# Performance work log

Hardware: AMD Instinct MI355X
Metric: run time of the kernel (lower is better)

Reference implementation:

```python
import jax, jax.numpy as jnp
import numpy as np

KS = 3
N = KS * KS  # 9 kernel taps
EPS = 1e-5
LEAK = 0.1


def _conv2d(x, w, b=None, stride=1, pad=1):
    out = jax.lax.conv_general_dilated(
        x, w, (stride, stride), [(pad, pad), (pad, pad)],
        dimension_numbers=('NCHW', 'OIHW', 'NCHW'))
    if b is not None:
        out = out + b[None, :, None, None]
    return out


def setup_inputs() -> dict:
    key = jax.random.key(0)
    k1, k2, k3, k4 = jax.random.split(key, 4)
    b, c_in, c_out, H, W = 4, 128, 256, 128, 128
    x = jax.random.normal(k1, (b, c_in, H, W), dtype=jnp.float32)
    # offset-predicting conv (torch inits it to zero; small random keeps
    # sampling near-grid but nontrivial)
    p_w = jax.random.normal(k2, (2 * N, c_in, KS, KS), dtype=jnp.float32) * 0.01
    p_b = jnp.zeros((2 * N,), dtype=jnp.float32)
    # main conv weight (bias=False in DeformConv2d)
    w_conv = jax.random.normal(k3, (c_out, c_in, KS, KS), dtype=jnp.float32) * 0.05
    gamma = jnp.ones((c_out,), dtype=jnp.float32)
    beta = jnp.zeros((c_out,), dtype=jnp.float32)
    return {"x": x, "p_w": p_w, "p_b": p_b, "w_conv": w_conv,
            "gamma": gamma, "beta": beta}


def reference(x, p_w, p_b, w_conv, gamma, beta):
    b, c, H, W = x.shape
    # offsets: (b, 2N, H, W); first N channels = x-offsets, last N = y-offsets
    off = jnp.transpose(_conv2d(x, p_w, p_b), (0, 2, 3, 1))  # (b,h,w,2N)
    off_x, off_y = off[..., :N], off[..., N:]

    x_pad = jnp.pad(x, ((0, 0), (0, 0), (1, 1), (1, 1)))  # zero_padding(1)
    Hp, Wp = H + 2, W + 2

    # p = p_0 + p_n + offset (in padded coordinates)
    dx = jnp.repeat(jnp.arange(-1, 2), KS).astype(x.dtype)  # (9,)
    dy = jnp.tile(jnp.arange(-1, 2), KS).astype(x.dtype)
    p0x = jnp.arange(1, H + 1, dtype=x.dtype)[None, :, None, None]
    p0y = jnp.arange(1, W + 1, dtype=x.dtype)[None, None, :, None]
    px = p0x + dx + off_x  # (b,h,w,N)
    py = p0y + dy + off_y

    fx, fy = jnp.floor(px), jnp.floor(py)
    qlt_x = jnp.clip(fx, 0, Hp - 1)
    qlt_y = jnp.clip(fy, 0, Wp - 1)
    qrb_x = jnp.clip(fx + 1, 0, Hp - 1)
    qrb_y = jnp.clip(fy + 1, 0, Wp - 1)

    pcx = jnp.clip(px, 0, Hp - 1)
    pcy = jnp.clip(py, 0, Wp - 1)

    # bilinear weights (matches original g_lt/g_rb/g_lb/g_rt)
    g_lt = (1 + (qlt_x - pcx)) * (1 + (qlt_y - pcy))
    g_rb = (1 - (qrb_x - pcx)) * (1 - (qrb_y - pcy))
    g_lb = (1 + (qlt_x - pcx)) * (1 - (qrb_y - pcy))
    g_rt = (1 - (qrb_x - pcx)) * (1 + (qlt_y - pcy))

    x_flat = x_pad.reshape(b, c, Hp * Wp)
    ilt_x, ilt_y = qlt_x.astype(jnp.int32), qlt_y.astype(jnp.int32)
    irb_x, irb_y = qrb_x.astype(jnp.int32), qrb_y.astype(jnp.int32)

    def samp(ix, iy, g):
        idx = (ix * Wp + iy).reshape(b, -1)  # (b, h*w*N)
        v = jnp.take_along_axis(x_flat, idx[:, None, :], axis=2)
        return g[:, None] * v.reshape(b, c, H, W, N)

    x_off = (samp(ilt_x, ilt_y, g_lt) + samp(irb_x, irb_y, g_rb)
             + samp(ilt_x, irb_y, g_lb) + samp(irb_x, ilt_y, g_rt))

    # equivalent to reshaping to (b,c,3h,3w) and conv(k=3,s=3), bias=False
    out = jnp.einsum('bchwn,ocn->bohw', x_off,
                     w_conv.reshape(w_conv.shape[0], c, N))

    # BatchNorm2d (training-mode batch stats, biased var) + LeakyReLU(0.1)
    mean = out.mean(axis=(0, 2, 3), keepdims=True)
    var = ((out - mean) ** 2).mean(axis=(0, 2, 3), keepdims=True)
    out = (out - mean) * jax.lax.rsqrt(var + EPS)
    out = out * gamma[None, :, None, None] + beta[None, :, None, None]
    return jnp.where(out >= 0, out, LEAK * out)
```

## Files before the change

kernel.cpp:

```cpp
#include <hip/hip_runtime.h>
#include <cstdint>

typedef __attribute__((ext_vector_type(8))) short bf16x8;
typedef __attribute__((ext_vector_type(4))) float f32x4;

#define B_   4
#define C_   128
#define H_   128
#define W_   128
#define HP_  130
#define WP_  130
#define O_   256
#define HW_  (H_*W_)

#define XPAD_BYTES   (B_*HP_*WP_*C_*2)
#define OFF_BYTE     XPAD_BYTES
#define OFF_BYTES    (B_*HW_*18*4)
#define WREPB_BYTE   (OFF_BYTE + OFF_BYTES)
#define WREPB_BYTES  (9*C_*O_*2)
#define STATS_BYTE   (WREPB_BYTE + WREPB_BYTES)
#define WOFF_BYTE    (STATS_BYTE + 4096)
#define WOFF_BYTES   (9*4*4*32*8*2)

typedef __attribute__((address_space(1))) const void gconst_void;
typedef __attribute__((address_space(3))) void lds_void;
#define GLD_LDS16(gp, lp) __builtin_amdgcn_global_load_lds((gconst_void*)(gp), (lds_void*)(lp), 16, 0, 0)

__device__ __forceinline__ unsigned pack_bf2(float a, float b) {
    unsigned ua = __builtin_bit_cast(unsigned, a) + 0x8000u;
    unsigned ub = __builtin_bit_cast(unsigned, b) + 0x8000u;
    return __builtin_amdgcn_perm(ub, ua, 0x07060302u);
}

__global__ void k_transpose(const float* __restrict__ x, unsigned short* __restrict__ xpad) {
    __shared__ float tile[32][33];
    int w0 = blockIdx.x * 32, c0 = blockIdx.y * 32;
    int bh = blockIdx.z;
    int b = bh >> 7, h = bh & 127;
    int tx = threadIdx.x, ty = threadIdx.y;
#pragma unroll
    for (int i = 0; i < 4; i++) {
        int c = c0 + ty + i * 8;
        tile[ty + i * 8][tx] = x[((b * C_ + c) * H_ + h) * W_ + w0 + tx];
    }
    int tid = ty * 32 + tx;
    if (h == 0) {
        int wloc = tid >> 3, cq = tid & 7;
        size_t r0 = ((size_t)(b * HP_ + 0)   * WP_ + (w0 + 1 + wloc)) * C_ + c0 + cq * 4;
        size_t r1 = ((size_t)(b * HP_ + 129) * WP_ + (w0 + 1 + wloc)) * C_ + c0 + cq * 4;
        *(uint2*)&xpad[r0] = make_uint2(0u, 0u);
        *(uint2*)&xpad[r1] = make_uint2(0u, 0u);
        if (w0 == 0 && tid < 128) {
            int corner = tid >> 5, cc = tid & 31;
            int hp = (corner & 1) ? 129 : 0;
            int wp = (corner & 2) ? 129 : 0;
            xpad[((size_t)(b * HP_ + hp) * WP_ + wp) * C_ + c0 + cc] = 0;
        }
    }
    if (w0 == 0 && tid < 64) {
        int side = tid >> 5, cc = tid & 31;
        int wp = side ? 129 : 0;
        xpad[((size_t)(b * HP_ + h + 1) * WP_ + wp) * C_ + c0 + cc] = 0;
    }
    __syncthreads();
    if (tid < 128) {
        int w = tid >> 2, u4 = tid & 3;
        unsigned r0 = pack_bf2(tile[8 * u4 + 0][w], tile[8 * u4 + 1][w]);
        unsigned r1 = pack_bf2(tile[8 * u4 + 2][w], tile[8 * u4 + 3][w]);
        unsigned r2 = pack_bf2(tile[8 * u4 + 4][w], tile[8 * u4 + 5][w]);
        unsigned r3 = pack_bf2(tile[8 * u4 + 6][w], tile[8 * u4 + 7][w]);
        *(uint4*)&xpad[((size_t)((b * HP_ + h + 1) * WP_ + (w0 + w + 1))) * C_ + c0 + u4 * 8] =
            make_uint4(r0, r1, r2, r3);
    }
}

__global__ void k_repackA(const float* __restrict__ p_w, short* __restrict__ wofff,
                          const float* __restrict__ w_conv, unsigned short* __restrict__ wrepb,
                          float* __restrict__ stats) {
    int i = blockIdx.x * 256 + threadIdx.x;
    if (i < 1024) stats[i] = 0.f;
    if (i < 9 * 4096) {
        int e = i & 7, m = (i >> 3) & 31, q = (i >> 8) & 3, kc = (i >> 10) & 3, tap = i >> 12;
        float f = (m < 18) ? p_w[((size_t)m * C_ + kc * 32 + q * 8 + e) * 9 + tap] : 0.f;
        unsigned u = __builtin_bit_cast(unsigned, f);
        u += 0x7fffu + ((u >> 16) & 1u);
        wofff[i] = (short)(u >> 16);
    }
    int j = i - 9 * 4096;
    if (j >= 0 && j < 9 * C_ * O_) {
        int ki8 = j & 7;
        int o   = (j >> 3) & 255;
        int kq  = (j >> 11) & 3;
        int kc  = (j >> 13) & 3;
        int n   = j >> 15;
        int c = kc * 32 + kq * 8 + ki8;
        float f = w_conv[(o * C_ + c) * 9 + n];
        unsigned u = __builtin_bit_cast(unsigned, f);
        u += 0x7fffu + ((u >> 16) & 1u);
        wrepb[j] = (unsigned short)(u >> 16);
    }
}

__global__ __launch_bounds__(256) void k_offconv(const unsigned short* __restrict__ xpad,
                                                 const short* __restrict__ wofff,
                                                 const float* __restrict__ p_b,
                                                 float* __restrict__ offT) {
    int t = threadIdx.x;
    int ph = blockIdx.x;
    int h  = blockIdx.y;
    int b  = blockIdx.z;
    const unsigned short* xb = xpad + (size_t)b * HP_ * WP_ * C_;
    int lane = t & 63, wv = t >> 6;
    int q = lane >> 4, l15 = lane & 15;
    int pos0 = ph * 64 + wv * 16;
    int poscol = pos0 + l15;

    f32x4 accA = {0.f, 0.f, 0.f, 0.f}, accB = {0.f, 0.f, 0.f, 0.f};
    const bf16x8* Wf = (const bf16x8*)wofff;

    for (int tap = 0; tap < 9; tap++) {
        int row = h + tap / 3;
        int col = poscol + tap % 3;
        const unsigned short* src = xb + ((size_t)(row * WP_ + col)) * C_ + q * 8;
#pragma unroll
        for (int kc = 0; kc < 4; kc++) {
            bf16x8 a0 = Wf[(size_t)(((tap * 4 + kc) * 4 + q) * 32) + l15];
            bf16x8 a1 = Wf[(size_t)(((tap * 4 + kc) * 4 + q) * 32) + 16 + l15];
            bf16x8 bv = *(const bf16x8*)(src + kc * 32);
            accA = __builtin_amdgcn_mfma_f32_16x16x32_bf16(a0, bv, accA, 0, 0, 0);
            accB = __builtin_amdgcn_mfma_f32_16x16x32_bf16(a1, bv, accB, 0, 0, 0);
        }
    }
    size_t hw = (size_t)h * W_ + pos0 + l15;
#pragma unroll
    for (int r = 0; r < 4; r++) {
        int j = q * 4 + r;
        offT[((size_t)(b * 18 + j)) * HW_ + hw] = accA[r] + p_b[j];
    }
    if (q == 0) {
#pragma unroll
        for (int r = 0; r < 2; r++) {
            int j = 16 + r;
            offT[((size_t)(b * 18 + j)) * HW_ + hw] = accB[r] + p_b[j];
        }
    }
}

__global__ __launch_bounds__(512, 4) void k_main(const unsigned short* __restrict__ xpad,
                                                 const float* __restrict__ offT,
                                                 const unsigned short* __restrict__ wrepb,
                                                 float* __restrict__ out,
                                                 float* __restrict__ stats) {
    __shared__ short Wl[2][8192];
    __shared__ short Vl[2][4128];
    __shared__ int   pbase[2][4][128];
    __shared__ float pg[2][4][128];
    __shared__ float red0[256], red1[256];

    int t = threadIdx.x;
    int i_blk = blockIdx.x;
    int b = i_blk & 3;
    int h = i_blk >> 2;
    const unsigned short* xb = xpad + (size_t)b * HP_ * WP_ * C_;

    int lane = t & 63, wv = t >> 6;
    int q = lane >> 4, l15 = lane & 15;
    int m0 = (wv & 3) * 64;
    int ph = wv >> 2;
    int n0 = ph * 64;
    int c4g = t & 3, posb = t >> 2;

    auto OFFSETS = [&](int n, int pb) {
        if (t < 128) {
            int w = t;
            float offx = offT[((size_t)(b * 18 + n)) * HW_ + h * W_ + w];
            float offy = offT[((size_t)(b * 18 + 9 + n)) * HW_ + h * W_ + w];
            int dxn = n / 3 - 1, dyn = n % 3 - 1;
            float px = (float)(h + 1 + dxn) + offx;
            float py = (float)(w + 1 + dyn) + offy;
            float pcx = fminf(fmaxf(px, 0.f), 129.f);
            float pcy = fminf(fmaxf(py, 0.f), 129.f);
            float fx = floorf(px), fy = floorf(py);
            float q0x = fminf(fmaxf(fx, 0.f), 129.f);
            float q0y = fminf(fmaxf(fy, 0.f), 129.f);
            float q1x = fminf(fmaxf(fx + 1.f, 0.f), 129.f);
            float q1y = fminf(fmaxf(fy + 1.f, 0.f), 129.f);
            float wx0 = 1.f + (q0x - pcx), wx1 = 1.f - (q1x - pcx);
            float wy0 = 1.f + (q0y - pcy), wy1 = 1.f - (q1y - pcy);
            int i0x = (int)q0x, i0y = (int)q0y, i1x = (int)q1x, i1y = (int)q1y;
            pbase[pb][0][w] = (i0x * WP_ + i0y) * C_;
            pbase[pb][1][w] = (i1x * WP_ + i1y) * C_;
            pbase[pb][2][w] = (i0x * WP_ + i1y) * C_;
            pbase[pb][3][w] = (i1x * WP_ + i0y) * C_;
            pg[pb][0][w] = wx0 * wy0;
            pg[pb][1][w] = wx1 * wy1;
            pg[pb][2][w] = wx0 * wy1;
            pg[pb][3][w] = wx1 * wy0;
        }
    };

    f32x4 acc[4][4];
#pragma unroll
    for (int i = 0; i < 4; i++)
#pragma unroll
        for (int j = 0; j < 4; j++) acc[i][j] = (f32x4){0.f, 0.f, 0.f, 0.f};

    if (t < 256) { red0[t] = 0.f; red1[t] = 0.f; }
    OFFSETS(0, 0);
    __syncthreads();

    {
        const unsigned short* ws = wrepb;
        GLD_LDS16(ws + (size_t)t * 8, &Wl[0][wv * 512]);
        GLD_LDS16(ws + (size_t)(t + 512) * 8, &Wl[0][wv * 512 + 4096]);
        int cof = c4g * 8;
        uint4 A  = *(const uint4*)(xb + pbase[0][0][posb] + cof);
        uint4 Bv = *(const uint4*)(xb + pbase[0][1][posb] + cof);
        uint4 Cv = *(const uint4*)(xb + pbase[0][2][posb] + cof);
        uint4 Dv = *(const uint4*)(xb + pbase[0][3][posb] + cof);
        float g0 = pg[0][0][posb], g1 = pg[0][1][posb], g2 = pg[0][2][posb], g3 = pg[0][3][posb];
        unsigned outw[4];
#pragma unroll
        for (int k = 0; k < 4; k++) {
            unsigned ua = (&A.x)[k], ub = (&Bv.x)[k], uc = (&Cv.x)[k], ud = (&Dv.x)[k];
            float alo = __builtin_bit_cast(float, ua << 16), ahi = __builtin_bit_cast(float, ua & 0xffff0000u);
            float blo = __builtin_bit_cast(float, ub << 16), bhi = __builtin_bit_cast(float, ub & 0xffff0000u);
            float clo = __builtin_bit_cast(float, uc << 16), chi = __builtin_bit_cast(float, uc & 0xffff0000u);
            float dlo = __builtin_bit_cast(float, ud << 16), dhi = __builtin_bit_cast(float, ud & 0xffff0000u);
            float vlo = g0 * alo + g1 * blo + g2 * clo + g3 * dlo;
            float vhi = g0 * ahi + g1 * bhi + g2 * chi + g3 * dhi;
            outw[k] = pack_bf2(vlo, vhi);
        }
        *(uint4*)&Vl[0][(unsigned)(c4g * 129 + posb) * 8] = make_uint4(outw[0], outw[1], outw[2], outw[3]);
    }
    __syncthreads();

#pragma unroll 1
    for (int s = 0; s < 36; s++) {
        int cur = s & 1, nxt = cur ^ 1;
        uint4 A, Bv, Cv, Dv;
        float g0 = 0.f, g1 = 0.f, g2 = 0.f, g3 = 0.f;
        bool st = (s < 35);
        if (st) {
            int s1 = s + 1;
            const unsigned short* ws = wrepb + (size_t)s1 * 8192;
            GLD_LDS16(ws + (size_t)t * 8, &Wl[nxt][wv * 512]);
            GLD_LDS16(ws + (size_t)(t + 512) * 8, &Wl[nxt][wv * 512 + 4096]);
            int n1 = s1 >> 2, kc1 = s1 & 3, pb1 = n1 & 1;
            int cof = kc1 * 32 + c4g * 8;
            A  = *(const uint4*)(xb + pbase[pb1][0][posb] + cof);
            Bv = *(const uint4*)(xb + pbase[pb1][1][posb] + cof);
            Cv = *(const uint4*)(xb + pbase[pb1][2][posb] + cof);
            Dv = *(const uint4*)(xb + pbase[pb1][3][posb] + cof);
            g0 = pg[pb1][0][posb]; g1 = pg[pb1][1][posb];
            g2 = pg[pb1][2][posb]; g3 = pg[pb1][3][posb];
        }
        {
            const bf16x8* Af = (const bf16x8*)Wl[cur];
            const bf16x8* Bf = (const bf16x8*)Vl[cur];
            bf16x8 av[4];
#pragma unroll
            for (int i = 0; i < 4; i++) av[i] = Af[q * 256 + m0 + i * 16 + l15];
            __builtin_amdgcn_s_setprio(1);
#pragma unroll
            for (int j = 0; j < 4; j++) {
                bf16x8 bv = Bf[q * 129 + n0 + j * 16 + l15];
#pragma unroll
                for (int i = 0; i < 4; i++)
                    acc[i][j] = __builtin_amdgcn_mfma_f32_16x16x32_bf16(av[i], bv, acc[i][j], 0, 0, 0);
            }
            __builtin_amdgcn_s_setprio(0);
        }
        if ((s & 3) == 2) {
            int n = s >> 2;
            if (n < 8) OFFSETS(n + 1, (n + 1) & 1);
        }
        if (st) {
            unsigned outw[4];
#pragma unroll
            for (int k = 0; k < 4; k++) {
                unsigned ua = (&A.x)[k], ub = (&Bv.x)[k], uc = (&Cv.x)[k], ud = (&Dv.x)[k];
                float alo = __builtin_bit_cast(float, ua << 16), ahi = __builtin_bit_cast(float, ua & 0xffff0000u);
                float blo = __builtin_bit_cast(float, ub << 16), bhi = __builtin_bit_cast(float, ub & 0xffff0000u);
                float clo = __builtin_bit_cast(float, uc << 16), chi = __builtin_bit_cast(float, uc & 0xffff0000u);
                float dlo = __builtin_bit_cast(float, ud << 16), dhi = __builtin_bit_cast(float, ud & 0xffff0000u);
                float vlo = g0 * alo + g1 * blo + g2 * clo + g3 * dlo;
                float vhi = g0 * ahi + g1 * bhi + g2 * chi + g3 * dhi;
                outw[k] = pack_bf2(vlo, vhi);
            }
            *(uint4*)&Vl[nxt][(unsigned)(c4g * 129 + posb) * 8] = make_uint4(outw[0], outw[1], outw[2], outw[3]);
        }
        __syncthreads();
    }

#pragma unroll
    for (int i = 0; i < 4; i++) {
#pragma unroll
        for (int r = 0; r < 4; r++) {
            int o_loc = m0 + i * 16 + q * 4 + r;
            float s = 0.f, s2 = 0.f;
#pragma unroll
            for (int j = 0; j < 4; j++) { float v = acc[i][j][r]; s += v; s2 += v * v; }
            s  += __shfl_xor(s, 1);  s  += __shfl_xor(s, 2);  s  += __shfl_xor(s, 4);  s  += __shfl_xor(s, 8);
            s2 += __shfl_xor(s2, 1); s2 += __shfl_xor(s2, 2); s2 += __shfl_xor(s2, 4); s2 += __shfl_xor(s2, 8);
            if (l15 == 0) { atomicAdd(&red0[o_loc], s); atomicAdd(&red1[o_loc], s2); }
        }
    }
    __syncthreads();
    if (t < 256) {
        atomicAdd(&stats[t], red0[t]);
        atomicAdd(&stats[256 + t], red1[t]);
    }

    float* outb = out + ((size_t)b * O_) * HW_ + (size_t)h * W_;
#pragma unroll
    for (int i = 0; i < 4; i++)
#pragma unroll
        for (int j = 0; j < 4; j++) {
            int col = ph * 64 + j * 16 + l15;
#pragma unroll
            for (int r = 0; r < 4; r++) {
                int o = m0 + i * 16 + q * 4 + r;
                outb[(size_t)o * HW_ + col] = acc[i][j][r];
            }
        }
}

__global__ __launch_bounds__(256) void k_apply(float* __restrict__ out,
                                               const float* __restrict__ stats,
                                               const float* __restrict__ gamma,
                                               const float* __restrict__ beta) {
    int idx = blockIdx.x * 256 + threadIdx.x;
    int e = idx * 4;
    int o = (e >> 14) & 255;
    float s0 = stats[o], s2v = stats[256 + o];
    float mean = s0 * (1.f / 65536.f);
    float var = s2v * (1.f / 65536.f) - mean * mean;
    float sc = gamma[o] * rsqrtf(var + 1e-5f);
    float sh = beta[o] - mean * sc;
    float4 v = *(float4*)(out + e);
    v.x = v.x * sc + sh; v.x = (v.x >= 0.f) ? v.x : 0.1f * v.x;
    v.y = v.y * sc + sh; v.y = (v.y >= 0.f) ? v.y : 0.1f * v.y;
    v.z = v.z * sc + sh; v.z = (v.z >= 0.f) ? v.z : 0.1f * v.z;
    v.w = v.w * sc + sh; v.w = (v.w >= 0.f) ? v.w : 0.1f * v.w;
    *(float4*)(out + e) = v;
}

extern "C" void kernel_launch(void* const* d_in, const int* in_sizes, int n_in,
                              void* d_out, int out_size, void* d_ws, size_t ws_size,
                              hipStream_t stream) {
    const float* x      = (const float*)d_in[0];
    const float* p_w    = (const float*)d_in[1];
    const float* p_b    = (const float*)d_in[2];
    const float* w_conv = (const float*)d_in[3];
    const float* gamma  = (const float*)d_in[4];
    const float* beta   = (const float*)d_in[5];
    float* out = (float*)d_out;

    char* wsb = (char*)d_ws;
    unsigned short* xpad  = (unsigned short*)wsb;
    float*          offT  = (float*)(wsb + OFF_BYTE);
    unsigned short* wrepb = (unsigned short*)(wsb + WREPB_BYTE);
    float*          stats = (float*)(wsb + STATS_BYTE);
    short*          wofff = (short*)(wsb + WOFF_BYTE);

    k_transpose<<<dim3(W_ / 32, C_ / 32, B_ * H_), dim3(32, 8), 0, stream>>>(x, xpad);
    k_repackA<<<dim3((9 * 4096 + 9 * C_ * O_ + 255) / 256), 256, 0, stream>>>(p_w, wofff, w_conv, wrepb, stats);
    k_offconv<<<dim3(2, H_, B_), 256, 0, stream>>>(xpad, wofff, p_b, offT);
    k_main<<<dim3(512), 512, 0, stream>>>(xpad, offT, wrepb, out, stats);
    k_apply<<<dim3(16384), 256, 0, stream>>>(out, stats, gamma, beta);
}
```

Before: 218.0 us.

## Store pre-norm conv output as bf16 and fold weight repack into transpose

The main kernel now writes its pre-normalization output to a bf16 scratch buffer when the workspace is large enough. A new apply kernel reads that buffer and writes the normalized fp32 result, so the intermediate round trip moves half the bytes of the fp32 read-modify-write. The weight repack and stats zeroing now run inside the transpose kernel, which removes one launch. The cost is bf16 rounding of the pre-BN values, and the zeroed stats must be visible before k_main runs, which holds because the two kernels are separate launches on the same stream.

```diff
diff --git a/kernel.cpp b/kernel.cpp
--- a/kernel.cpp
+++ b/kernel.cpp
@@ -21,6 +21,9 @@
 #define STATS_BYTE   (WREPB_BYTE + WREPB_BYTES)
 #define WOFF_BYTE    (STATS_BYTE + 4096)
 #define WOFF_BYTES   (9*4*4*32*8*2)
+#define RAW_BYTE     (WOFF_BYTE + WOFF_BYTES)
+#define RAW_BYTES    ((size_t)B_*O_*HW_*2)
+#define WS_NEED      ((size_t)RAW_BYTE + RAW_BYTES)
 
 typedef __attribute__((address_space(1))) const void gconst_void;
 typedef __attribute__((address_space(3))) void lds_void;
@@ -32,7 +35,16 @@
     return __builtin_amdgcn_perm(ub, ua, 0x07060302u);
 }
 
-__global__ void k_transpose(const float* __restrict__ x, unsigned short* __restrict__ xpad) {
+__device__ __forceinline__ unsigned short bf16_rne(float f) {
+    unsigned u = __builtin_bit_cast(unsigned, f);
+    u += 0x7fffu + ((u >> 16) & 1u);
+    return (unsigned short)(u >> 16);
+}
+
+__global__ void k_transpose(const float* __restrict__ x, unsigned short* __restrict__ xpad,
+                            const float* __restrict__ p_w, short* __restrict__ wofff,
+                            const float* __restrict__ w_conv, unsigned short* __restrict__ wrepb,
+                            float* __restrict__ stats) {
     __shared__ float tile[32][33];
     int w0 = blockIdx.x * 32, c0 = blockIdx.y * 32;
     int bh = blockIdx.z;
@@ -44,6 +56,26 @@
         tile[ty + i * 8][tx] = x[((b * C_ + c) * H_ + h) * W_ + w0 + tx];
     }
     int tid = ty * 32 + tx;
+    {
+        int fb = (bh * 4 + (int)blockIdx.y) * 4 + (int)blockIdx.x;
+        int i = fb * 256 + tid;
+        if (i < 1024) stats[i] = 0.f;
+        if (i < 9 * 4096) {
+            int e = i & 7, m = (i >> 3) & 31, q = (i >> 8) & 3, kc = (i >> 10) & 3, tap = i >> 12;
+            float f = (m < 18) ? p_w[((size_t)m * C_ + kc * 32 + q * 8 + e) * 9 + tap] : 0.f;
+            wofff[i] = (short)bf16_rne(f);
+        }
+        int j = i - 9 * 4096;
+        if (j >= 0 && j < 9 * C_ * O_) {
+            int ki8 = j & 7;
+            int o   = (j >> 3) & 255;
+            int kq  = (j >> 11) & 3;
+            int kc  = (j >> 13) & 3;
+            int n   = j >> 15;
+            int c = kc * 32 + kq * 8 + ki8;
+            wrepb[j] = bf16_rne(w_conv[(o * C_ + c) * 9 + n]);
+        }
+    }
     if (h == 0) {
         int wloc = tid >> 3, cq = tid & 7;
         size_t r0 = ((size_t)(b * HP_ + 0)   * WP_ + (w0 + 1 + wloc)) * C_ + c0 + cq * 4;
@@ -71,33 +103,6 @@
         unsigned r3 = pack_bf2(tile[8 * u4 + 6][w], tile[8 * u4 + 7][w]);
         *(uint4*)&xpad[((size_t)((b * HP_ + h + 1) * WP_ + (w0 + w + 1))) * C_ + c0 + u4 * 8] =
             make_uint4(r0, r1, r2, r3);
-    }
-}
-
-__global__ void k_repackA(const float* __restrict__ p_w, short* __restrict__ wofff,
-                          const float* __restrict__ w_conv, unsigned short* __restrict__ wrepb,
-                          float* __restrict__ stats) {
-    int i = blockIdx.x * 256 + threadIdx.x;
-    if (i < 1024) stats[i] = 0.f;
-    if (i < 9 * 4096) {
-        int e = i & 7, m = (i >> 3) & 31, q = (i >> 8) & 3, kc = (i >> 10) & 3, tap = i >> 12;
-        float f = (m < 18) ? p_w[((size_t)m * C_ + kc * 32 + q * 8 + e) * 9 + tap] : 0.f;
-        unsigned u = __builtin_bit_cast(unsigned, f);
-        u += 0x7fffu + ((u >> 16) & 1u);
-        wofff[i] = (short)(u >> 16);
-    }
-    int j = i - 9 * 4096;
-    if (j >= 0 && j < 9 * C_ * O_) {
-        int ki8 = j & 7;
-        int o   = (j >> 3) & 255;
-        int kq  = (j >> 11) & 3;
-        int kc  = (j >> 13) & 3;
-        int n   = j >> 15;
-        int c = kc * 32 + kq * 8 + ki8;
-        float f = w_conv[(o * C_ + c) * 9 + n];
-        unsigned u = __builtin_bit_cast(unsigned, f);
-        u += 0x7fffu + ((u >> 16) & 1u);
-        wrepb[j] = (unsigned short)(u >> 16);
     }
 }
 
@@ -150,7 +155,9 @@
                                                  const float* __restrict__ offT,
                                                  const unsigned short* __restrict__ wrepb,
                                                  float* __restrict__ out,
-                                                 float* __restrict__ stats) {
+                                                 float* __restrict__ stats,
+                                                 unsigned short* __restrict__ rawout,
+                                                 int bf16flag) {
     __shared__ short Wl[2][8192];
     __shared__ short Vl[2][4128];
     __shared__ int   pbase[2][4][128];
@@ -312,24 +319,69 @@
         atomicAdd(&stats[256 + t], red1[t]);
     }
 
-    float* outb = out + ((size_t)b * O_) * HW_ + (size_t)h * W_;
-#pragma unroll
-    for (int i = 0; i < 4; i++)
-#pragma unroll
-        for (int j = 0; j < 4; j++) {
-            int col = ph * 64 + j * 16 + l15;
-#pragma unroll
-            for (int r = 0; r < 4; r++) {
-                int o = m0 + i * 16 + q * 4 + r;
-                outb[(size_t)o * HW_ + col] = acc[i][j][r];
+    if (bf16flag) {
+        unsigned short* rb = rawout + ((size_t)b * O_) * HW_ + (size_t)h * W_;
+#pragma unroll
+        for (int i = 0; i < 4; i++)
+#pragma unroll
+            for (int j = 0; j < 4; j++) {
+                int col = ph * 64 + j * 16 + l15;
+#pragma unroll
+                for (int r = 0; r < 4; r++) {
+                    int o = m0 + i * 16 + q * 4 + r;
+                    rb[(size_t)o * HW_ + col] = bf16_rne(acc[i][j][r]);
+                }
             }
-        }
-}
-
-__global__ __launch_bounds__(256) void k_apply(float* __restrict__ out,
-                                               const float* __restrict__ stats,
-                                               const float* __restrict__ gamma,
-                                               const float* __restrict__ beta) {
+    } else {
+        float* outb = out + ((size_t)b * O_) * HW_ + (size_t)h * W_;
+#pragma unroll
+        for (int i = 0; i < 4; i++)
+#pragma unroll
+            for (int j = 0; j < 4; j++) {
+                int col = ph * 64 + j * 16 + l15;
+#pragma unroll
+                for (int r = 0; r < 4; r++) {
+                    int o = m0 + i * 16 + q * 4 + r;
+                    outb[(size_t)o * HW_ + col] = acc[i][j][r];
+                }
+            }
+    }
+}
+
+__global__ __launch_bounds__(256) void k_apply_bf16(const unsigned short* __restrict__ raw,
+                                                    float* __restrict__ out,
+                                                    const float* __restrict__ stats,
+                                                    const float* __restrict__ gamma,
+                                                    const float* __restrict__ beta) {
+    size_t idx = (size_t)blockIdx.x * 256 + threadIdx.x;
+    size_t e = idx * 8;
+    int o = (int)((e >> 14) & 255);
+    float s0 = stats[o], s2v = stats[256 + o];
+    float mean = s0 * (1.f / 65536.f);
+    float var = s2v * (1.f / 65536.f) - mean * mean;
+    float sc = gamma[o] * rsqrtf(var + 1e-5f);
+    float sh = beta[o] - mean * sc;
+    uint4 rv = *(const uint4*)(raw + e);
+    float vo[8];
+#pragma unroll
+    for (int k = 0; k < 4; k++) {
+        unsigned w = (&rv.x)[k];
+        vo[2 * k]     = __builtin_bit_cast(float, w << 16);
+        vo[2 * k + 1] = __builtin_bit_cast(float, w & 0xffff0000u);
+    }
+#pragma unroll
+    for (int k = 0; k < 8; k++) {
+        float v = vo[k] * sc + sh;
+        vo[k] = (v >= 0.f) ? v : 0.1f * v;
+    }
+    *(float4*)(out + e)     = make_float4(vo[0], vo[1], vo[2], vo[3]);
+    *(float4*)(out + e + 4) = make_float4(vo[4], vo[5], vo[6], vo[7]);
+}
+
+__global__ __launch_bounds__(256) void k_apply_f32(float* __restrict__ out,
+                                                   const float* __restrict__ stats,
+                                                   const float* __restrict__ gamma,
+                                                   const float* __restrict__ beta) {
     int idx = blockIdx.x * 256 + threadIdx.x;
     int e = idx * 4;
     int o = (e >> 14) & 255;
@@ -363,10 +415,16 @@
     unsigned short* wrepb = (unsigned short*)(wsb + WREPB_BYTE);
     float*          stats = (float*)(wsb + STATS_BYTE);
     short*          wofff = (short*)(wsb + WOFF_BYTE);
-
-    k_transpose<<<dim3(W_ / 32, C_ / 32, B_ * H_), dim3(32, 8), 0, stream>>>(x, xpad);
-    k_repackA<<<dim3((9 * 4096 + 9 * C_ * O_ + 255) / 256), 256, 0, stream>>>(p_w, wofff, w_conv, wrepb, stats);
+    unsigned short* rawo  = (unsigned short*)(wsb + RAW_BYTE);
+
+    int bf16flag = (ws_size >= WS_NEED) ? 1 : 0;
+
+    k_transpose<<<dim3(W_ / 32, C_ / 32, B_ * H_), dim3(32, 8), 0, stream>>>(
+        x, xpad, p_w, wofff, w_conv, wrepb, stats);
     k_offconv<<<dim3(2, H_, B_), 256, 0, stream>>>(xpad, wofff, p_b, offT);
-    k_main<<<dim3(512), 512, 0, stream>>>(xpad, offT, wrepb, out, stats);
-    k_apply<<<dim3(16384), 256, 0, stream>>>(out, stats, gamma, beta);
-}
+    k_main<<<dim3(512), 512, 0, stream>>>(xpad, offT, wrepb, out, stats, rawo, bf16flag);
+    if (bf16flag)
+        k_apply_bf16<<<dim3(B_ * O_ * HW_ / (256 * 8)), 256, 0, stream>>>(rawo, out, stats, gamma, beta);
+    else
+        k_apply_f32<<<dim3(B_ * O_ * HW_ / (256 * 4)), 256, 0, stream>>>(out, stats, gamma, beta);
+}
```

New measurement: 214.9 us. About the same (-1.4%).
